# Kernel optimization log

Measured on AMD Instinct MI355X. Metric: run time of the kernel, lower is better.

Reference implementation:

```python
import jax, jax.numpy as jnp
import numpy as np

NORM_DISP_RANGE = np.linspace(0.0, 0.3, 24).astype(np.float32)  # D=24 disparity planes
TRAIN_W = 640  # train_image_size[1]


def _conv1x1(x, w, b=None):
    # x: [B,C,H,W], w: [O,C]
    y = jnp.einsum('bchw,oc->bohw', x, w)
    if b is not None:
        y = y + b[None, :, None, None]
    return y


def _l2norm(x, eps=1e-12):
    # F.normalize(dim=1)
    n = jnp.sqrt(jnp.sum(x * x, axis=1, keepdims=True))
    return x / jnp.maximum(n, eps)


def _warp_stack(k, directs, rel_scale):
    """Plane-sweep warp: shift k horizontally by each disparity (grid_sample
    bilinear, border padding, align_corners=True). Only x is displaced, so the
    bilinear sample reduces to a 1-D lerp along W.  Returns [B,C,H,W,D]."""
    B, C, H, W = k.shape
    disp = jnp.asarray(NORM_DISP_RANGE, k.dtype)  # [D]
    xs = jnp.arange(W, dtype=k.dtype)             # pixel x coords (align_corners)
    # normalized shift disp*2*rel_scale*direct -> pixels: *(W-1)/2
    shift = disp[None, :] * 2.0 * rel_scale * directs.reshape(B, 1) * (W - 1) / 2.0  # [B,D]
    ix = jnp.clip(xs[None, :, None] + shift[:, None, :], 0.0, W - 1)  # [B,W,D] (border clamp)
    ix0 = jnp.floor(ix).astype(jnp.int32)
    ix1 = jnp.minimum(ix0 + 1, W - 1)
    w1 = (ix - ix0.astype(k.dtype))[:, None, None, :, :]  # [B,1,1,W,D]

    def gather(kb, i0, i1):  # kb: [C,H,W], i0/i1: [W,D]
        return kb[:, :, i0], kb[:, :, i1]  # [C,H,W,D]

    g0, g1 = jax.vmap(gather)(k, ix0, ix1)
    return g0 * (1.0 - w1) + g1 * w1


def setup_inputs() -> dict:
    key = jax.random.key(0)
    ks = jax.random.split(key, 16)
    B, C, H, W = 4, 128, 96, 320
    Cr = C // 4
    s = 0.05
    directs = jnp.sign(jax.random.normal(ks[2], (B, 1, 1, 1), jnp.float32) + 1e-6)
    return {
        't_feat': jax.random.normal(ks[0], (B, C, H, W), jnp.float32),
        's_feat': jax.random.normal(ks[1], (B, C, H, W), jnp.float32),
        'directs': directs,
        'image_shape': jnp.array([B, 3, 384, 1280], jnp.int32),
        'q_w': jax.random.normal(ks[3], (Cr, C), jnp.float32) * s,
        'q_b': jax.random.normal(ks[4], (Cr,), jnp.float32) * s,
        'k_w': jax.random.normal(ks[5], (Cr, C), jnp.float32) * s,
        'k_b': jax.random.normal(ks[6], (Cr,), jnp.float32) * s,
        'ce_w': jax.random.normal(ks[7], (C, Cr), jnp.float32) * s,
        'ce_b': jax.random.normal(ks[8], (C,), jnp.float32) * s,
        'fa_w': jax.random.normal(ks[9], (1, 2 * C), jnp.float32) * s,
        'fa_b': jax.random.normal(ks[10], (1,), jnp.float32) * s,
        'redu_w': jax.random.normal(ks[11], (C, C, 3, 3), jnp.float32) * s,
        'se_w1': jax.random.normal(ks[12], (C // 16, C), jnp.float32) * s,
        'se_w2': jax.random.normal(ks[13], (C, C // 16), jnp.float32) * s,
    }


def reference(t_feat, s_feat, directs, image_shape, q_w, q_b, k_w, k_b,
              ce_w, ce_b, fa_w, fa_b, redu_w, se_w1, se_w2):
    rel_scale = jnp.asarray(TRAIN_W, t_feat.dtype) / image_shape[3].astype(t_feat.dtype)
    q = _l2norm(_conv1x1(t_feat, q_w, q_b))     # [B,Cr,H,W]
    k = _l2norm(_conv1x1(s_feat, k_w, k_b))
    warped = _warp_stack(k, directs, rel_scale)  # [B,Cr,H,W,D]
    sim = jnp.einsum('bchw,bchwd->bhwd', q, warped)
    prob = jax.nn.softmax(sim, axis=-1)          # softmax over disparity
    cost = jnp.einsum('bchwd,bhwd->bchw', warped, prob)
    cost_exp = _conv1x1(cost, ce_w, ce_b)        # [B,C,H,W]
    alpha = jax.nn.sigmoid(_conv1x1(jnp.concatenate([t_feat, cost_exp], axis=1), fa_w, fa_b))
    fused = alpha * t_feat + (1.0 - alpha) * cost_exp
    # redu: reflect-pad 3x3 conv (no bias) -> SE -> ELU
    xp = jnp.pad(fused, ((0, 0), (0, 0), (1, 1), (1, 1)), mode='reflect')
    conv = jax.lax.conv_general_dilated(xp, redu_w, (1, 1), 'VALID',
                                        dimension_numbers=('NCHW', 'OIHW', 'NCHW'))
    pooled = jnp.mean(conv, axis=(2, 3))  # [B,C]
    gate = jax.nn.sigmoid(jnp.einsum('br,cr->bc', jax.nn.relu(jnp.einsum('bc,rc->br', pooled, se_w1)), se_w2))
    out = jax.nn.elu(conv * gate[:, :, None, None])
    prob_out = jnp.transpose(prob, (0, 3, 1, 2))  # [B,D,H,W] as in torch
    return out, prob_out
```

## Files before the change

### kernel.cpp

```cpp
#include <hip/hip_runtime.h>
#include <math.h>

#define BB 4
#define CC 128
#define CRR 32
#define DD 24
#define HH 96
#define WW 320
#define HWW (HH*WW)

typedef __attribute__((ext_vector_type(8))) short bs8;
typedef __attribute__((ext_vector_type(4))) float f32x4;
typedef __attribute__((ext_vector_type(4))) int   i32x4;

static __device__ __forceinline__ unsigned short f2bf(float x) {
    unsigned int u = __float_as_uint(x);
    unsigned int r = (u + 0x7fffu + ((u >> 16) & 1u)) >> 16;
    return (unsigned short)r;
}

__global__ __launch_bounds__(256) void repack_all_kernel(
    const float* __restrict__ q_w, const float* __restrict__ k_w,
    const float* __restrict__ ce_w, const float* __restrict__ redu_w,
    unsigned short* __restrict__ wqk, unsigned short* __restrict__ wce,
    unsigned short* __restrict__ wb)
{
    int idx = blockIdx.x * 256 + threadIdx.x;
    if (idx < 8192) {
        int j   = idx & 7;
        int l   = (idx >> 3) & 63;
        int kc  = (idx >> 9) & 3;
        int ofh = (idx >> 11) & 1;
        int g   = idx >> 12;
        const float* w = g ? k_w : q_w;
        int oc = ofh * 16 + (l & 15);
        int ic = kc * 32 + (l >> 4) * 8 + j;
        wqk[idx] = f2bf(w[oc * CC + ic]);
    } else if (idx < 12288) {
        int i   = idx - 8192;
        int j   = i & 7;
        int l   = (i >> 3) & 63;
        int ofg = (i >> 9) & 7;
        int oc = ofg * 16 + (l & 15);
        int ic = (l >> 4) * 8 + j;
        wce[i] = f2bf(ce_w[oc * CRR + ic]);
    } else {
        int i2 = idx - 12288;
        int j    = i2 & 7;
        int l    = (i2 >> 3) & 63;
        int rest = i2 >> 9;
        int ocf  = rest & 7;
        int kc   = (rest >> 3) & 3;
        int tap  = rest >> 5;
        int oc = ocf * 16 + (l & 15);
        int ic = kc * 32 + (l >> 4) * 8 + j;
        wb[i2] = f2bf(redu_w[(size_t)(oc * CC + ic) * 9 + tap]);
    }
}

__global__ __launch_bounds__(256) void qk_mfma_kernel(
    const float* __restrict__ t_feat, const float* __restrict__ s_feat,
    const unsigned short* __restrict__ wqk,
    const float* __restrict__ q_b, const float* __restrict__ k_b,
    float* __restrict__ ws_q, float* __restrict__ ws_k)
{
    __shared__ __align__(16) unsigned char lds[2 * 64 * 16 * 16];
    int tid  = threadIdx.x;
    int lane = tid & 63;
    int wid  = __builtin_amdgcn_readfirstlane(tid >> 6);
    int g = wid >> 1, ofh = wid & 1;
    int p0 = blockIdx.x * 64;
    int b = p0 / HWW, rem0 = p0 % HWW;

    for (int ci = tid; ci < 2 * 64 * 16; ci += 256) {
        int px   = ci & 63;
        int slot = (ci >> 6) & 15;
        int m    = ci >> 10;
        const float* src = (m ? s_feat : t_feat)
                         + (size_t)b * CC * HWW + (size_t)(slot * 8) * HWW + rem0 + px;
        i32x4 u;
        #pragma unroll
        for (int j = 0; j < 4; ++j) {
            unsigned short lo = f2bf(src[(size_t)(2 * j) * HWW]);
            unsigned short hi = f2bf(src[(size_t)(2 * j + 1) * HWW]);
            u[j] = (int)((unsigned int)lo | ((unsigned int)hi << 16));
        }
        int addr = m * 16384 + px * 256 + ((slot ^ (px & 7)) << 4);
        *(i32x4*)(lds + addr) = u;
    }
    __syncthreads();

    int l15 = lane & 15, l4 = lane >> 4;
    f32x4 acc[4];
    #pragma unroll
    for (int pf = 0; pf < 4; ++pf) acc[pf] = (f32x4){0.f, 0.f, 0.f, 0.f};

    const bs8* wp = (const bs8*)wqk + (size_t)(g * 2 + ofh) * 4 * 64;
    #pragma unroll
    for (int kc = 0; kc < 4; ++kc) {
        bs8 bf = wp[kc * 64 + lane];
        #pragma unroll
        for (int pf = 0; pf < 4; ++pf) {
            int addr = g * 16384 + (pf * 16 + l15) * 256 + (((kc * 4 + l4) ^ (l15 & 7)) << 4);
            bs8 a = *(const bs8*)(lds + addr);
            acc[pf] = __builtin_amdgcn_mfma_f32_16x16x32_bf16(bf, a, acc[pf], 0, 0, 0);
        }
    }

    float4 bias4 = *(const float4*)((g ? k_b : q_b) + ofh * 16 + l4 * 4);
    float np[4];
    #pragma unroll
    for (int pf = 0; pf < 4; ++pf) {
        float s = 0.f;
        #pragma unroll
        for (int r = 0; r < 4; ++r) {
            float v = acc[pf][r] + ((const float*)&bias4)[r];
            acc[pf][r] = v;
            s = fmaf(v, v, s);
        }
        s += __shfl_xor(s, 16, 64);
        s += __shfl_xor(s, 32, 64);
        np[pf] = s;
    }
    __syncthreads();
    float* fl = (float*)lds;
    if (l4 == 0) {
        #pragma unroll
        for (int pf = 0; pf < 4; ++pf)
            fl[(g * 2 + ofh) * 64 + pf * 16 + l15] = np[pf];
    }
    __syncthreads();

    float* dst = (g ? ws_k : ws_q) + ((size_t)b * HWW + rem0) * CRR;
    #pragma unroll
    for (int pf = 0; pf < 4; ++pf) {
        int px = pf * 16 + l15;
        float tot = fl[(g * 2) * 64 + px] + fl[(g * 2 + 1) * 64 + px];
        float inv = 1.f / fmaxf(sqrtf(tot), 1e-12f);
        float4 v;
        v.x = acc[pf][0] * inv; v.y = acc[pf][1] * inv;
        v.z = acc[pf][2] * inv; v.w = acc[pf][3] * inv;
        *(float4*)(dst + (size_t)px * CRR + ofh * 16 + l4 * 4) = v;
    }
}

#define SC_TILE 64
#define SC_NCOLS 114
__global__ __launch_bounds__(256) void simcost_kernel(
    const float* __restrict__ directs, const int* __restrict__ image_shape,
    const float* __restrict__ ws_q, const float* __restrict__ ws_k,
    float* __restrict__ prob_out, float* __restrict__ ws_cost)
{
    __shared__ __align__(16) unsigned char kl[SC_NCOLS * 128];
    int tid = threadIdx.x;
    int b = blockIdx.z, h = blockIdx.y, w0 = blockIdx.x * SC_TILE;

    float rel = 640.0f / (float)image_shape[3];
    float fscale = rel * directs[b] * (float)(WW - 1);
    int base = (fscale >= 0.f) ? w0 : (w0 - 49);

    const float* krow = ws_k + ((size_t)b * HWW + h * WW) * CRR;
    for (int i = tid; i < SC_NCOLS * 8; i += 256) {
        int col = i >> 3, j = i & 7;
        int gc = min(max(base + col, 0), WW - 1);
        float4 v = *(const float4*)(krow + (size_t)gc * CRR + j * 4);
        *(float4*)(kl + col * 128 + ((j ^ (col & 7)) << 4)) = v;
    }
    __syncthreads();

    int quarter = tid & 3;
    int pxl = tid >> 2;
    int w = w0 + pxl;
    int rem = h * WW + w;
    size_t p = (size_t)b * HWW + rem;

    float4 q0, q1;
    {
        const float4* qb = (const float4*)(ws_q + p * CRR + quarter * 8);
        q0 = qb[0]; q1 = qb[1];
    }

    float e[DD];
    float Z = 0.f;
    float4 c0 = {0.f,0.f,0.f,0.f}, c1 = {0.f,0.f,0.f,0.f};
    int j0 = quarter * 2, j1 = quarter * 2 + 1;

    #pragma unroll
    for (int d = 0; d < DD; ++d) {
        float disp = 0.3f * (float)d / 23.0f;
        float fx = fminf(fmaxf((float)w + disp * fscale, 0.f), (float)(WW - 1));
        int ix0 = (int)floorf(fx);
        int ix1 = min(ix0 + 1, WW - 1);
        float w1 = fx - (float)ix0;
        int ca = ix0 - base, cb2 = ix1 - base;
        float4 a0 = *(const float4*)(kl + ca  * 128 + ((j0 ^ (ca  & 7)) << 4));
        float4 a1 = *(const float4*)(kl + ca  * 128 + ((j1 ^ (ca  & 7)) << 4));
        float4 b0 = *(const float4*)(kl + cb2 * 128 + ((j0 ^ (cb2 & 7)) << 4));
        float4 b1 = *(const float4*)(kl + cb2 * 128 + ((j1 ^ (cb2 & 7)) << 4));
        float4 w0v, w1v;
        w0v.x = fmaf(w1, b0.x - a0.x, a0.x);
        w0v.y = fmaf(w1, b0.y - a0.y, a0.y);
        w0v.z = fmaf(w1, b0.z - a0.z, a0.z);
        w0v.w = fmaf(w1, b0.w - a0.w, a0.w);
        w1v.x = fmaf(w1, b1.x - a1.x, a1.x);
        w1v.y = fmaf(w1, b1.y - a1.y, a1.y);
        w1v.z = fmaf(w1, b1.z - a1.z, a1.z);
        w1v.w = fmaf(w1, b1.w - a1.w, a1.w);
        float s = 0.f;
        s = fmaf(q0.x, w0v.x, s); s = fmaf(q0.y, w0v.y, s);
        s = fmaf(q0.z, w0v.z, s); s = fmaf(q0.w, w0v.w, s);
        s = fmaf(q1.x, w1v.x, s); s = fmaf(q1.y, w1v.y, s);
        s = fmaf(q1.z, w1v.z, s); s = fmaf(q1.w, w1v.w, s);
        s += __shfl_xor(s, 1, 64);
        s += __shfl_xor(s, 2, 64);
        float ee = __expf(s);
        e[d] = ee;
        Z += ee;
        c0.x = fmaf(ee, w0v.x, c0.x); c0.y = fmaf(ee, w0v.y, c0.y);
        c0.z = fmaf(ee, w0v.z, c0.z); c0.w = fmaf(ee, w0v.w, c0.w);
        c1.x = fmaf(ee, w1v.x, c1.x); c1.y = fmaf(ee, w1v.y, c1.y);
        c1.z = fmaf(ee, w1v.z, c1.z); c1.w = fmaf(ee, w1v.w, c1.w);
    }
    float inv = 1.f / Z;
    if (quarter == 0) {
        #pragma unroll
        for (int d = 0; d < DD; ++d)
            prob_out[((size_t)b * DD + d) * HWW + rem] = e[d] * inv;
    }
    c0.x *= inv; c0.y *= inv; c0.z *= inv; c0.w *= inv;
    c1.x *= inv; c1.y *= inv; c1.z *= inv; c1.w *= inv;
    float4* cb = (float4*)(ws_cost + p * CRR + quarter * 8);
    cb[0] = c0; cb[1] = c1;
}

__global__ __launch_bounds__(256) void fuse_mfma_kernel(
    const float* __restrict__ t_feat, const unsigned short* __restrict__ wce,
    const float* __restrict__ ce_b, const float* __restrict__ fa_w,
    const float* __restrict__ fa_b,
    const float* __restrict__ ws_cost, unsigned short* __restrict__ fused)
{
    __shared__ __align__(16) unsigned char ldsA[64 * 64];
    __shared__ float lds_pa[64][4];
    __shared__ float lds_alpha[64];
    int tid  = threadIdx.x;
    int lane = tid & 63;
    int wid  = __builtin_amdgcn_readfirstlane(tid >> 6);
    int p0 = blockIdx.x * 64;
    int b = p0 / HWW, rem0 = p0 % HWW;

    {
        int px = tid & 63, slot = tid >> 6;
        const float* src = ws_cost + (size_t)(p0 + px) * CRR + slot * 8;
        i32x4 u;
        #pragma unroll
        for (int j = 0; j < 4; ++j) {
            unsigned short lo = f2bf(src[2 * j]);
            unsigned short hi = f2bf(src[2 * j + 1]);
            u[j] = (int)((unsigned int)lo | ((unsigned int)hi << 16));
        }
        int addr = px * 64 + ((slot ^ (px & 3)) << 4);
        *(i32x4*)(ldsA + addr) = u;
    }
    __syncthreads();

    int l15 = lane & 15, l4 = lane >> 4;
    f32x4 acc[4][2];
    #pragma unroll
    for (int pf = 0; pf < 4; ++pf)
        #pragma unroll
        for (int of = 0; of < 2; ++of)
            acc[pf][of] = (f32x4){0.f, 0.f, 0.f, 0.f};

    const bs8* wp = (const bs8*)wce;
    #pragma unroll
    for (int pf = 0; pf < 4; ++pf) {
        int row = pf * 16 + l15;
        bs8 a = *(const bs8*)(ldsA + row * 64 + ((l4 ^ (l15 & 3)) << 4));
        #pragma unroll
        for (int of = 0; of < 2; ++of) {
            bs8 bf = wp[(wid * 2 + of) * 64 + lane];
            acc[pf][of] = __builtin_amdgcn_mfma_f32_16x16x32_bf16(bf, a, acc[pf][of], 0, 0, 0);
        }
    }

    const float* tb = t_feat + (size_t)b * CC * HWW + rem0;
    float tv[4][2][4];
    float pa[4];
    #pragma unroll
    for (int pf = 0; pf < 4; ++pf) pa[pf] = 0.f;

    #pragma unroll
    for (int of = 0; of < 2; ++of) {
        int ocb = wid * 32 + of * 16 + l4 * 4;
        float4 cb4 = *(const float4*)(ce_b + ocb);
        float4 f14 = *(const float4*)(fa_w + ocb);
        float4 f24 = *(const float4*)(fa_w + CC + ocb);
        #pragma unroll
        for (int pf = 0; pf < 4; ++pf) {
            int px = pf * 16 + l15;
            #pragma unroll
            for (int r = 0; r < 4; ++r) {
                float ce = acc[pf][of][r] + ((const float*)&cb4)[r];
                acc[pf][of][r] = ce;
                float t = tb[(size_t)(ocb + r) * HWW + px];
                tv[pf][of][r] = t;
                pa[pf] = fmaf(((const float*)&f14)[r], t,
                              fmaf(((const float*)&f24)[r], ce, pa[pf]));
            }
        }
    }
    #pragma unroll
    for (int pf = 0; pf < 4; ++pf) {
        float v = pa[pf];
        v += __shfl_xor(v, 16, 64);
        v += __shfl_xor(v, 32, 64);
        if (l4 == 0) lds_pa[pf * 16 + l15][wid] = v;
    }
    __syncthreads();
    if (tid < 64) {
        float s = lds_pa[tid][0] + lds_pa[tid][1] + lds_pa[tid][2] + lds_pa[tid][3] + fa_b[0];
        lds_alpha[tid] = 1.f / (1.f + expf(-s));
    }
    __syncthreads();

    #pragma unroll
    for (int pf = 0; pf < 4; ++pf) {
        int px = pf * 16 + l15;
        float alpha = lds_alpha[px];
        unsigned short* dst = fused + (size_t)(p0 + px) * CC;
        #pragma unroll
        for (int of = 0; of < 2; ++of) {
            int ocb = wid * 32 + of * 16 + l4 * 4;
            float v0 = alpha * tv[pf][of][0] + (1.f - alpha) * acc[pf][of][0];
            float v1 = alpha * tv[pf][of][1] + (1.f - alpha) * acc[pf][of][1];
            float v2 = alpha * tv[pf][of][2] + (1.f - alpha) * acc[pf][of][2];
            float v3 = alpha * tv[pf][of][3] + (1.f - alpha) * acc[pf][of][3];
            uint2 u;
            u.x = (unsigned int)f2bf(v0) | ((unsigned int)f2bf(v1) << 16);
            u.y = (unsigned int)f2bf(v2) | ((unsigned int)f2bf(v3) << 16);
            *(uint2*)(dst + ocb) = u;
        }
    }
}

__global__ __launch_bounds__(256, 6) void conv_mfma_kernel(
    const unsigned short* __restrict__ fused, const unsigned short* __restrict__ wb,
    float* __restrict__ out_conv, float* __restrict__ pool_partial)
{
    __shared__ __align__(16) unsigned char lds[3 * 66 * 128];
    int tid  = threadIdx.x;
    int lane = tid & 63;
    int wid  = __builtin_amdgcn_readfirstlane(tid >> 6);
    int w0 = blockIdx.x * 64;
    int h  = blockIdx.y;
    int b  = blockIdx.z;

    const unsigned short* fb = fused + (size_t)b * HWW * CC;

    int l15 = lane & 15, l4 = lane >> 4;
    const bs8* wbp = (const bs8*)wb;

    f32x4 acc[4][2];
    #pragma unroll
    for (int pf = 0; pf < 4; ++pf)
        #pragma unroll
        for (int of = 0; of < 2; ++of)
            acc[pf][of] = (f32x4){0.f, 0.f, 0.f, 0.f};

    int basex[3], xr6[3][2];
    #pragma unroll
    for (int kx = 0; kx < 3; ++kx) {
        basex[kx] = (l15 + kx) * 128;
        #pragma unroll
        for (int kcl = 0; kcl < 2; ++kcl)
            xr6[kx][kcl] = ((kcl * 4 + l4) ^ ((l15 + kx) & 7)) << 4;
    }

    #pragma unroll
    for (int p = 0; p < 2; ++p) {
        if (p > 0) __syncthreads();
        for (int ci = tid; ci < 3 * 66 * 8; ci += 256) {
            int row  = ci / 528;
            int r2   = ci - row * 528;
            int col  = r2 >> 3;
            int slot = r2 & 7;
            int grow = h - 1 + row; grow = grow < 0 ? 1 : (grow > HH - 1 ? HH - 2 : grow);
            int gcol = w0 - 1 + col; gcol = gcol < 0 ? -gcol : (gcol > WW - 1 ? 2 * (WW - 1) - gcol : gcol);
            i32x4 u = *(const i32x4*)(fb + (size_t)(grow * WW + gcol) * CC + p * 64 + slot * 8);
            *(i32x4*)(lds + (row * 66 + col) * 128 + ((slot ^ (col & 7)) << 4)) = u;
        }
        __syncthreads();

        #pragma unroll
        for (int ky = 0; ky < 3; ++ky) {
            #pragma unroll
            for (int kx = 0; kx < 3; ++kx) {
                int tap = ky * 3 + kx;
                #pragma unroll
                for (int kcl = 0; kcl < 2; ++kcl) {
                    int kcg = p * 2 + kcl;
                    bs8 a[4];
                    #pragma unroll
                    for (int pf = 0; pf < 4; ++pf)
                        a[pf] = *(const bs8*)(lds + ky * 8448 + pf * 2048
                                              + basex[kx] + xr6[kx][kcl]);
                    bs8 bf0 = wbp[((tap * 4 + kcg) * 8 + wid * 2 + 0) * 64 + lane];
                    bs8 bf1 = wbp[((tap * 4 + kcg) * 8 + wid * 2 + 1) * 64 + lane];
                    #pragma unroll
                    for (int pf = 0; pf < 4; ++pf) {
                        acc[pf][0] = __builtin_amdgcn_mfma_f32_16x16x32_bf16(bf0, a[pf], acc[pf][0], 0, 0, 0);
                        acc[pf][1] = __builtin_amdgcn_mfma_f32_16x16x32_bf16(bf1, a[pf], acc[pf][1], 0, 0, 0);
                    }
                }
            }
        }
    }

    #pragma unroll
    for (int pf = 0; pf < 4; ++pf) {
        int px = pf * 16 + l15;
        #pragma unroll
        for (int of = 0; of < 2; ++of) {
            #pragma unroll
            for (int r = 0; r < 4; ++r) {
                int oc = wid * 32 + of * 16 + l4 * 4 + r;
                out_conv[((size_t)b * CC + oc) * HWW + h * WW + w0 + px] = acc[pf][of][r];
            }
        }
    }

    int blk = h * (WW / 64) + blockIdx.x;
    #pragma unroll
    for (int of = 0; of < 2; ++of) {
        #pragma unroll
        for (int r = 0; r < 4; ++r) {
            float v = acc[0][of][r] + acc[1][of][r] + acc[2][of][r] + acc[3][of][r];
            v += __shfl_xor(v, 1, 64);
            v += __shfl_xor(v, 2, 64);
            v += __shfl_xor(v, 4, 64);
            v += __shfl_xor(v, 8, 64);
            if (l15 == 0) {
                int oc = wid * 32 + of * 16 + l4 * 4 + r;
                pool_partial[((size_t)b * CC + oc) * 480 + blk] = v;
            }
        }
    }
}

__global__ __launch_bounds__(256) void pool_kernel(
    const float* __restrict__ partial, float* __restrict__ pool)
{
    int plane = blockIdx.x;
    const float* p = partial + (size_t)plane * 480;
    float s = 0.f;
    for (int i = threadIdx.x; i < 480; i += 256) s += p[i];
    #pragma unroll
    for (int off = 32; off; off >>= 1) s += __shfl_down(s, off);
    __shared__ float wsum[4];
    if ((threadIdx.x & 63) == 0) wsum[threadIdx.x >> 6] = s;
    __syncthreads();
    if (threadIdx.x == 0)
        pool[plane] = (wsum[0] + wsum[1] + wsum[2] + wsum[3]) / (float)HWW;
}

__global__ __launch_bounds__(256) void segate_kernel(
    const float* __restrict__ pool, const float* __restrict__ w1,
    const float* __restrict__ w2, float* __restrict__ gate)
{
    __shared__ float hidden[BB * 8];
    int t = threadIdx.x;
    if (t < BB * 8) {
        int b = t / 8, r = t % 8;
        float s = 0.f;
        for (int c = 0; c < CC; ++c) s = fmaf(pool[b * CC + c], w1[r * CC + c], s);
        hidden[t] = fmaxf(s, 0.f);
    }
    __syncthreads();
    for (int idx = t; idx < BB * CC; idx += 256) {
        int b = idx / CC, c = idx % CC;
        float s = 0.f;
        #pragma unroll
        for (int r = 0; r < 8; ++r) s = fmaf(hidden[b * 8 + r], w2[c * 8 + r], s);
        gate[idx] = 1.f / (1.f + expf(-s));
    }
}

__global__ __launch_bounds__(256) void elu_kernel(
    float* __restrict__ out, const float* __restrict__ gate)
{
    size_t i4 = ((size_t)blockIdx.x * 256 + threadIdx.x) * 4;
    int plane = (int)(i4 / HWW);
    float g = gate[plane];
    float4 v = *(float4*)(out + i4);
    v.x *= g; v.y *= g; v.z *= g; v.w *= g;
    v.x = v.x > 0.f ? v.x : expm1f(v.x);
    v.y = v.y > 0.f ? v.y : expm1f(v.y);
    v.z = v.z > 0.f ? v.z : expm1f(v.z);
    v.w = v.w > 0.f ? v.w : expm1f(v.w);
    *(float4*)(out + i4) = v;
}

extern "C" void kernel_launch(void* const* d_in, const int* in_sizes, int n_in,
                              void* d_out, int out_size, void* d_ws, size_t ws_size,
                              hipStream_t stream)
{
    (void)in_sizes; (void)n_in; (void)out_size; (void)ws_size;
    const float* t_feat      = (const float*)d_in[0];
    const float* s_feat      = (const float*)d_in[1];
    const float* directs     = (const float*)d_in[2];
    const int*   image_shape = (const int*)d_in[3];
    const float* q_w  = (const float*)d_in[4];
    const float* q_b  = (const float*)d_in[5];
    const float* k_w  = (const float*)d_in[6];
    const float* k_b  = (const float*)d_in[7];
    const float* ce_w = (const float*)d_in[8];
    const float* ce_b = (const float*)d_in[9];
    const float* fa_w = (const float*)d_in[10];
    const float* fa_b = (const float*)d_in[11];
    const float* redu_w = (const float*)d_in[12];
    const float* se_w1  = (const float*)d_in[13];
    const float* se_w2  = (const float*)d_in[14];

    float* out      = (float*)d_out;
    float* prob_out = out + (size_t)BB * CC * HWW;

    const size_t QK = (size_t)BB * CRR * HWW;
    const size_t F  = (size_t)BB * CC * HWW;
    float* ws       = (float*)d_ws;
    float* ws_q     = ws;
    float* ws_k     = ws + QK;
    float* ws_cost  = ws_q;
    unsigned short* ws_fused = (unsigned short*)(ws + 2 * QK);
    float* ws_partial = ws + 2 * QK + F / 2;
    unsigned short* ws_wce = (unsigned short*)(ws_partial + (size_t)BB * CC * 480);
    unsigned short* ws_wb  = ws_wce + 4096;
    float* ws_pool  = ws + 2 * QK + F;
    float* ws_gate  = ws_pool + BB * CC;
    unsigned short* ws_wqk = (unsigned short*)ws_fused;

    repack_all_kernel<<<624, 256, 0, stream>>>(q_w, k_w, ce_w, redu_w,
                                               ws_wqk, ws_wce, ws_wb);
    qk_mfma_kernel<<<BB * HWW / 64, 256, 0, stream>>>(t_feat, s_feat, ws_wqk,
                                                      q_b, k_b, ws_q, ws_k);
    simcost_kernel<<<dim3(WW / SC_TILE, HH, BB), 256, 0, stream>>>(
        directs, image_shape, ws_q, ws_k, prob_out, ws_cost);
    fuse_mfma_kernel<<<BB * HWW / 64, 256, 0, stream>>>(t_feat, ws_wce, ce_b, fa_w, fa_b,
                                                        ws_cost, ws_fused);
    conv_mfma_kernel<<<dim3(WW / 64, HH, BB), 256, 0, stream>>>(ws_fused, ws_wb, out, ws_partial);
    pool_kernel<<<BB * CC, 256, 0, stream>>>(ws_partial, ws_pool);
    segate_kernel<<<1, 256, 0, stream>>>(ws_pool, se_w1, se_w2, ws_gate);
    elu_kernel<<<(BB * CC * HWW) / 1024, 256, 0, stream>>>(out, ws_gate);
}
```

Measured before the change: 180.0 us.

## Compute two output rows per conv block and store conv intermediate as bf16

The 3x3 conv kernel now computes two output rows per block, so each loaded weight fragment and the shared halo rows serve twice as many MFMAs, and the grid halves. The conv result is written to a bf16 scratch buffer instead of the fp32 output, and the ELU/gate kernel reads bf16 and writes fp32. The goal is less global traffic for the conv intermediate and fewer redundant weight and halo loads. In exchange, register pressure rises (accumulators double, occupancy hint lowered from 6 to 4), and rounding the pre-activation to bf16 adds error.

```diff
diff --git a/kernel.cpp b/kernel.cpp
--- a/kernel.cpp
+++ b/kernel.cpp
@@ -8,15 +8,20 @@
 #define HH 96
 #define WW 320
 #define HWW (HH*WW)
+#define NBLK 240
 
 typedef __attribute__((ext_vector_type(8))) short bs8;
 typedef __attribute__((ext_vector_type(4))) float f32x4;
 typedef __attribute__((ext_vector_type(4))) int   i32x4;
+typedef __attribute__((ext_vector_type(8))) short s8v;
 
 static __device__ __forceinline__ unsigned short f2bf(float x) {
     unsigned int u = __float_as_uint(x);
     unsigned int r = (u + 0x7fffu + ((u >> 16) & 1u)) >> 16;
     return (unsigned short)r;
+}
+static __device__ __forceinline__ float bf2f(unsigned short u) {
+    return __uint_as_float(((unsigned int)u) << 16);
 }
 
 __global__ __launch_bounds__(256) void repack_all_kernel(
@@ -343,16 +348,16 @@
     }
 }
 
-__global__ __launch_bounds__(256, 6) void conv_mfma_kernel(
+__global__ __launch_bounds__(256, 4) void conv_mfma_kernel(
     const unsigned short* __restrict__ fused, const unsigned short* __restrict__ wb,
-    float* __restrict__ out_conv, float* __restrict__ pool_partial)
-{
-    __shared__ __align__(16) unsigned char lds[3 * 66 * 128];
+    unsigned short* __restrict__ conv_bf16, float* __restrict__ pool_partial)
+{
+    __shared__ __align__(16) unsigned char lds[4 * 66 * 128];
     int tid  = threadIdx.x;
     int lane = tid & 63;
     int wid  = __builtin_amdgcn_readfirstlane(tid >> 6);
     int w0 = blockIdx.x * 64;
-    int h  = blockIdx.y;
+    int h0 = blockIdx.y * 2;
     int b  = blockIdx.z;
 
     const unsigned short* fb = fused + (size_t)b * HWW * CC;
@@ -360,12 +365,14 @@
     int l15 = lane & 15, l4 = lane >> 4;
     const bs8* wbp = (const bs8*)wb;
 
-    f32x4 acc[4][2];
-    #pragma unroll
-    for (int pf = 0; pf < 4; ++pf)
-        #pragma unroll
-        for (int of = 0; of < 2; ++of)
-            acc[pf][of] = (f32x4){0.f, 0.f, 0.f, 0.f};
+    f32x4 acc[2][4][2];
+    #pragma unroll
+    for (int ri = 0; ri < 2; ++ri)
+        #pragma unroll
+        for (int pf = 0; pf < 4; ++pf)
+            #pragma unroll
+            for (int of = 0; of < 2; ++of)
+                acc[ri][pf][of] = (f32x4){0.f, 0.f, 0.f, 0.f};
 
     int basex[3], xr6[3][2];
     #pragma unroll
@@ -379,12 +386,12 @@
     #pragma unroll
     for (int p = 0; p < 2; ++p) {
         if (p > 0) __syncthreads();
-        for (int ci = tid; ci < 3 * 66 * 8; ci += 256) {
+        for (int ci = tid; ci < 4 * 66 * 8; ci += 256) {
             int row  = ci / 528;
             int r2   = ci - row * 528;
             int col  = r2 >> 3;
             int slot = r2 & 7;
-            int grow = h - 1 + row; grow = grow < 0 ? 1 : (grow > HH - 1 ? HH - 2 : grow);
+            int grow = h0 - 1 + row; grow = grow < 0 ? 1 : (grow > HH - 1 ? HH - 2 : grow);
             int gcol = w0 - 1 + col; gcol = gcol < 0 ? -gcol : (gcol > WW - 1 ? 2 * (WW - 1) - gcol : gcol);
             i32x4 u = *(const i32x4*)(fb + (size_t)(grow * WW + gcol) * CC + p * 64 + slot * 8);
             *(i32x4*)(lds + (row * 66 + col) * 128 + ((slot ^ (col & 7)) << 4)) = u;
@@ -399,17 +406,18 @@
                 #pragma unroll
                 for (int kcl = 0; kcl < 2; ++kcl) {
                     int kcg = p * 2 + kcl;
-                    bs8 a[4];
-                    #pragma unroll
-                    for (int pf = 0; pf < 4; ++pf)
-                        a[pf] = *(const bs8*)(lds + ky * 8448 + pf * 2048
-                                              + basex[kx] + xr6[kx][kcl]);
                     bs8 bf0 = wbp[((tap * 4 + kcg) * 8 + wid * 2 + 0) * 64 + lane];
                     bs8 bf1 = wbp[((tap * 4 + kcg) * 8 + wid * 2 + 1) * 64 + lane];
                     #pragma unroll
-                    for (int pf = 0; pf < 4; ++pf) {
-                        acc[pf][0] = __builtin_amdgcn_mfma_f32_16x16x32_bf16(bf0, a[pf], acc[pf][0], 0, 0, 0);
-                        acc[pf][1] = __builtin_amdgcn_mfma_f32_16x16x32_bf16(bf1, a[pf], acc[pf][1], 0, 0, 0);
+                    for (int ri = 0; ri < 2; ++ri) {
+                        int sr = ri + ky;
+                        #pragma unroll
+                        for (int pf = 0; pf < 4; ++pf) {
+                            bs8 a = *(const bs8*)(lds + sr * 8448 + pf * 2048
+                                                  + basex[kx] + xr6[kx][kcl]);
+                            acc[ri][pf][0] = __builtin_amdgcn_mfma_f32_16x16x32_bf16(bf0, a, acc[ri][pf][0], 0, 0, 0);
+                            acc[ri][pf][1] = __builtin_amdgcn_mfma_f32_16x16x32_bf16(bf1, a, acc[ri][pf][1], 0, 0, 0);
+                        }
                     }
                 }
             }
@@ -417,32 +425,40 @@
     }
 
     #pragma unroll
-    for (int pf = 0; pf < 4; ++pf) {
-        int px = pf * 16 + l15;
-        #pragma unroll
-        for (int of = 0; of < 2; ++of) {
+    for (int ri = 0; ri < 2; ++ri) {
+        #pragma unroll
+        for (int pf = 0; pf < 4; ++pf) {
+            int px = pf * 16 + l15;
             #pragma unroll
-            for (int r = 0; r < 4; ++r) {
-                int oc = wid * 32 + of * 16 + l4 * 4 + r;
-                out_conv[((size_t)b * CC + oc) * HWW + h * WW + w0 + px] = acc[pf][of][r];
+            for (int of = 0; of < 2; ++of) {
+                #pragma unroll
+                for (int r = 0; r < 4; ++r) {
+                    int oc = wid * 32 + of * 16 + l4 * 4 + r;
+                    conv_bf16[((size_t)b * CC + oc) * HWW + (h0 + ri) * WW + w0 + px] =
+                        f2bf(acc[ri][pf][of][r]);
+                }
             }
         }
     }
 
-    int blk = h * (WW / 64) + blockIdx.x;
+    int blk = blockIdx.y * 5 + blockIdx.x;
+    float* pp = pool_partial + ((size_t)b * NBLK + blk) * CC;
     #pragma unroll
     for (int of = 0; of < 2; ++of) {
         #pragma unroll
         for (int r = 0; r < 4; ++r) {
-            float v = acc[0][of][r] + acc[1][of][r] + acc[2][of][r] + acc[3][of][r];
+            float v = 0.f;
+            #pragma unroll
+            for (int ri = 0; ri < 2; ++ri)
+                #pragma unroll
+                for (int pf = 0; pf < 4; ++pf)
+                    v += acc[ri][pf][of][r];
             v += __shfl_xor(v, 1, 64);
             v += __shfl_xor(v, 2, 64);
             v += __shfl_xor(v, 4, 64);
             v += __shfl_xor(v, 8, 64);
-            if (l15 == 0) {
-                int oc = wid * 32 + of * 16 + l4 * 4 + r;
-                pool_partial[((size_t)b * CC + oc) * 480 + blk] = v;
-            }
+            if (l15 == 0)
+                pp[wid * 32 + of * 16 + l4 * 4 + r] = v;
         }
     }
 }
@@ -451,9 +467,10 @@
     const float* __restrict__ partial, float* __restrict__ pool)
 {
     int plane = blockIdx.x;
-    const float* p = partial + (size_t)plane * 480;
+    int b = plane >> 7, c = plane & 127;
     float s = 0.f;
-    for (int i = threadIdx.x; i < 480; i += 256) s += p[i];
+    for (int i = threadIdx.x; i < NBLK; i += 256)
+        s += partial[((size_t)b * NBLK + i) * CC + c];
     #pragma unroll
     for (int off = 32; off; off >>= 1) s += __shfl_down(s, off);
     __shared__ float wsum[4];
@@ -486,18 +503,21 @@
 }
 
 __global__ __launch_bounds__(256) void elu_kernel(
-    float* __restrict__ out, const float* __restrict__ gate)
-{
-    size_t i4 = ((size_t)blockIdx.x * 256 + threadIdx.x) * 4;
-    int plane = (int)(i4 / HWW);
+    const unsigned short* __restrict__ conv_bf16, const float* __restrict__ gate,
+    float* __restrict__ out)
+{
+    size_t base = ((size_t)blockIdx.x * 256 + threadIdx.x) * 8;
+    int plane = (int)(base / HWW);
     float g = gate[plane];
-    float4 v = *(float4*)(out + i4);
-    v.x *= g; v.y *= g; v.z *= g; v.w *= g;
-    v.x = v.x > 0.f ? v.x : expm1f(v.x);
-    v.y = v.y > 0.f ? v.y : expm1f(v.y);
-    v.z = v.z > 0.f ? v.z : expm1f(v.z);
-    v.w = v.w > 0.f ? v.w : expm1f(v.w);
-    *(float4*)(out + i4) = v;
+    s8v v = *(const s8v*)(conv_bf16 + base);
+    float o[8];
+    #pragma unroll
+    for (int j = 0; j < 8; ++j) {
+        float x = bf2f((unsigned short)v[j]) * g;
+        o[j] = x > 0.f ? x : expm1f(x);
+    }
+    *(float4*)(out + base)     = (float4){o[0], o[1], o[2], o[3]};
+    *(float4*)(out + base + 4) = (float4){o[4], o[5], o[6], o[7]};
 }
 
 extern "C" void kernel_launch(void* const* d_in, const int* in_sizes, int n_in,
@@ -530,9 +550,10 @@
     float* ws_q     = ws;
     float* ws_k     = ws + QK;
     float* ws_cost  = ws_q;
+    unsigned short* ws_convb = (unsigned short*)ws;
     unsigned short* ws_fused = (unsigned short*)(ws + 2 * QK);
     float* ws_partial = ws + 2 * QK + F / 2;
-    unsigned short* ws_wce = (unsigned short*)(ws_partial + (size_t)BB * CC * 480);
+    unsigned short* ws_wce = (unsigned short*)(ws_partial + (size_t)BB * NBLK * CC);
     unsigned short* ws_wb  = ws_wce + 4096;
     float* ws_pool  = ws + 2 * QK + F;
     float* ws_gate  = ws_pool + BB * CC;
@@ -546,8 +567,9 @@
         directs, image_shape, ws_q, ws_k, prob_out, ws_cost);
     fuse_mfma_kernel<<<BB * HWW / 64, 256, 0, stream>>>(t_feat, ws_wce, ce_b, fa_w, fa_b,
                                                         ws_cost, ws_fused);
-    conv_mfma_kernel<<<dim3(WW / 64, HH, BB), 256, 0, stream>>>(ws_fused, ws_wb, out, ws_partial);
+    conv_mfma_kernel<<<dim3(WW / 64, HH / 2, BB), 256, 0, stream>>>(ws_fused, ws_wb,
+                                                                    ws_convb, ws_partial);
     pool_kernel<<<BB * CC, 256, 0, stream>>>(ws_partial, ws_pool);
     segate_kernel<<<1, 256, 0, stream>>>(ws_pool, se_w1, se_w2, ws_gate);
-    elu_kernel<<<(BB * CC * HWW) / 1024, 256, 0, stream>>>(out, ws_gate);
-}
+    elu_kernel<<<(BB * CC * HWW) / 2048, 256, 0, stream>>>(ws_convb, ws_gate, out);
+}
```

Result: slower. 260.0 us (+44.5%).
